# Optimization experiments

Hardware: AMD Instinct MI355X
Metric: run time of the kernel (lower is better)

The kernel has to match this reference:

```python
import jax, jax.numpy as jnp
import numpy as np
from jax import lax

B, T, H, Q = 32, 2000, 896, 256
SUB = H // 2


def wavrnn_normalize(x):
    return 2.0 * x / 255.0 - 1.0


def setup_inputs() -> dict:
    key = jax.random.key(0)
    ks = jax.random.split(key, 10)
    p = lambda k, shape: (jax.random.normal(k, shape, dtype=jnp.float32) * 0.02)
    return {
        "sample": jax.random.randint(ks[0], (B, T, 2), 0, 256, dtype=jnp.int32),
        "cts": jax.random.randint(ks[1], (B, T, 1), 0, 256, dtype=jnp.int32),
        "state": jnp.zeros((B, H), dtype=jnp.float32),
        "R": p(ks[2], (3 * H, H)),
        "Wc": p(ks[3], (3 * SUB, 2)),
        "Wf": p(ks[4], (3 * SUB, 3)),
        "b_u": jnp.zeros((H,), jnp.float32),
        "b_r": jnp.zeros((H,), jnp.float32),
        "b_e": jnp.zeros((H,), jnp.float32),
        "Wc1": p(ks[5], (SUB, SUB)),
        "bc1": jnp.zeros((SUB,), jnp.float32),
        "Wc2": p(ks[6], (Q, SUB)),
        "bc2": jnp.zeros((Q,), jnp.float32),
        "Wf1": p(ks[7], (SUB, SUB)),
        "bf1": jnp.zeros((SUB,), jnp.float32),
        "Wf2": p(ks[8], (Q, SUB)),
        "bf2": jnp.zeros((Q,), jnp.float32),
    }


def reference(sample, cts, state, R, Wc, Wf, b_u, b_r, b_e,
              Wc1, bc1, Wc2, bc2, Wf1, bf1, Wf2, bf2):
    s = wavrnn_normalize(sample.astype(jnp.float32))          # [B,T,2]
    c = wavrnn_normalize(cts.astype(jnp.float32))             # [B,T,1]
    s_f = jnp.concatenate([s, c], axis=2)                     # [B,T,3]

    proj_c = jnp.einsum('btk,ok->bto', s, Wc)                 # [B,T,3*SUB]
    proj_f = jnp.einsum('btk,ok->bto', s_f, Wf)               # [B,T,3*SUB]
    utc, rtc, etc_ = jnp.split(proj_c, 3, axis=2)
    utf, rtf, etf = jnp.split(proj_f, 3, axis=2)
    fwd_u = jnp.concatenate([utc, utf], axis=2)               # [B,T,H]
    fwd_r = jnp.concatenate([rtc, rtf], axis=2)
    fwd_e = jnp.concatenate([etc_, etf], axis=2)

    # time-major for scan: [T,B,H]
    xs = (jnp.swapaxes(fwd_u, 0, 1), jnp.swapaxes(fwd_r, 0, 1), jnp.swapaxes(fwd_e, 0, 1))

    def step(h, x):
        fu, fr, fe = x                                        # each [B,H]
        r_ = h @ R.T                                          # [B,3H]
        r_u, r_r, r_e = jnp.split(r_, 3, axis=1)
        ut = jax.nn.sigmoid(r_u + fu + b_u)
        rt = jax.nn.sigmoid(r_r + fr + b_r)
        et = jnp.tanh(rt * r_e + fe + b_e)
        h_new = ut * h + (1.0 - ut) * et
        return h_new, h_new

    last, states = lax.scan(step, state, xs)                  # states [T,B,H]
    states = jnp.swapaxes(states, 0, 1)                       # [B,T,H]
    htc, htf = jnp.split(states, 2, axis=2)                   # [B,T,SUB] each

    ct = jax.nn.log_softmax(
        jax.nn.relu(jnp.einsum('btk,ok->bto', htc, Wc1) + bc1) @ Wc2.T + bc2, axis=2)
    ft = jax.nn.log_softmax(
        jax.nn.relu(jnp.einsum('btk,ok->bto', htf, Wf1) + bf1) @ Wf2.T + bf2, axis=2)
    return (ct, ft, last[:, None, :])
```

## Files before the change

### kernel.cpp

```cpp
#include <hip/hip_runtime.h>
#include <hip/hip_bf16.h>

#define B_   32
#define T_   2000
#define H_   896
#define SUB_ 448
#define Q_   256

#define FT_OFF   16384000
#define LAST_OFF 32768000

#define NBLK_ 28

#define WS_FLAGS  0
#define WS_H0     8192
#define WS_WB     65536
#define WS_STATES 1327104

#define WB_W1C 0
#define WB_W1F 200704
#define WB_W2C 401408
#define WB_W2F 516096
#define WB_N   630784

#define SLOT_B 57344
#define SLOT_E 28672

typedef __attribute__((ext_vector_type(8)))  short bf16x8;
typedef __attribute__((ext_vector_type(16))) float f32x16;

__device__ __forceinline__ unsigned short f2bf(float f) {
    unsigned int u = __builtin_bit_cast(unsigned int, f);
    u += 0x7fff + ((u >> 16) & 1);
    return (unsigned short)(u >> 16);
}
__device__ __forceinline__ float bf2f(unsigned short u) {
    return __builtin_bit_cast(float, (unsigned int)u << 16);
}
__device__ __forceinline__ void gload_lds16(const void* g, void* l) {
    __builtin_amdgcn_global_load_lds(
        (const __attribute__((address_space(1))) unsigned int*)g,
        (__attribute__((address_space(3))) unsigned int*)l, 16, 0, 0);
}
__device__ __forceinline__ bf16x8 mk8(short4 a, short4 b) {
    bf16x8 f;
    f[0]=a.x; f[1]=a.y; f[2]=a.z; f[3]=a.w;
    f[4]=b.x; f[5]=b.y; f[6]=b.z; f[7]=b.w;
    return f;
}
__device__ __forceinline__ float fsig(float x) {
    return __builtin_amdgcn_rcpf(1.0f + __expf(-x));
}
__device__ __forceinline__ float ftanh(float x) {
    float xc = fminf(fmaxf(x, -9.0f), 9.0f);
    float z  = __expf(2.0f * xc);
    return 1.0f - 2.0f * __builtin_amdgcn_rcpf(z + 1.0f);
}

__global__ void wavrnn_prep(const float* __restrict__ state,
                            const float* __restrict__ Wc1, const float* __restrict__ Wf1,
                            const float* __restrict__ Wc2, const float* __restrict__ Wf2,
                            unsigned short* __restrict__ wb,
                            unsigned short* __restrict__ h0,
                            int* __restrict__ flags) {
    const int i = blockIdx.x * 256 + threadIdx.x;
    if (i < WB_N) {
        float v;
        if      (i < WB_W1F) v = Wc1[i];
        else if (i < WB_W2C) v = Wf1[i - WB_W1F];
        else if (i < WB_W2F) v = Wc2[i - WB_W2C];
        else                 v = Wf2[i - WB_W2F];
        wb[i] = f2bf(v);
    }
    if (i < 64) flags[i] = 0;
    if (i < B_ * H_) h0[i] = f2bf(state[i]);
}

__global__ __launch_bounds__(192, 1)
void wavrnn_scan8(const int* __restrict__ sample, const int* __restrict__ cts,
                  const float* __restrict__ state, const float* __restrict__ R,
                  const float* __restrict__ Wc, const float* __restrict__ Wf,
                  const float* __restrict__ b_u, const float* __restrict__ b_r,
                  const float* __restrict__ b_e,
                  const unsigned short* __restrict__ h0,
                  int* __restrict__ flags,
                  unsigned short* __restrict__ states,
                  float* __restrict__ out)
{
    const int tid  = (int)threadIdx.x;
    const int w    = tid >> 6;
    const int lane = tid & 63;
    const int s31  = lane & 31;
    const int hi   = lane >> 5;
    const int b    = (int)blockIdx.x;

    __shared__ __align__(16) char Abuf[32 * 2048];
    __shared__ float gate_out[3][32][34];

    const int jgB = b * 32 + s31;
    bf16x8 Bf[56];
    {
        const float* Rrow = R + (size_t)(w * H_ + jgB) * H_;
        #pragma unroll
        for (int c = 0; c < 56; ++c) {
            const float4 p0 = *(const float4*)(Rrow + 16*c + 4*hi);
            const float4 p1 = *(const float4*)(Rrow + 16*c + 8 + 4*hi);
            bf16x8 f;
            f[0]=(short)f2bf(p0.x); f[1]=(short)f2bf(p0.y);
            f[2]=(short)f2bf(p0.z); f[3]=(short)f2bf(p0.w);
            f[4]=(short)f2bf(p1.x); f[5]=(short)f2bf(p1.y);
            f[6]=(short)f2bf(p1.z); f[7]=(short)f2bf(p1.w);
            Bf[c] = f;
        }
    }

    const int jp  = tid & 15;
    const int sg  = (tid >> 4) & 7;
    const int j0  = 2 * jp;
    const int jg0 = b * 32 + j0;
    float wu[2][3], wr[2][3], we[2][3], gb[2][3];
    float hreg[4][2];
    if (tid < 128) {
        #pragma unroll
        for (int jj = 0; jj < 2; ++jj) {
            const int jg = jg0 + jj;
            if (jg < SUB_) {
                wu[jj][0]=Wc[2*jg];            wu[jj][1]=Wc[2*jg+1];            wu[jj][2]=0.f;
                wr[jj][0]=Wc[2*(SUB_+jg)];     wr[jj][1]=Wc[2*(SUB_+jg)+1];     wr[jj][2]=0.f;
                we[jj][0]=Wc[2*(2*SUB_+jg)];   we[jj][1]=Wc[2*(2*SUB_+jg)+1];   we[jj][2]=0.f;
            } else {
                const int jf = jg - SUB_;
                wu[jj][0]=Wf[3*jf];            wu[jj][1]=Wf[3*jf+1];            wu[jj][2]=Wf[3*jf+2];
                wr[jj][0]=Wf[3*(SUB_+jf)];     wr[jj][1]=Wf[3*(SUB_+jf)+1];     wr[jj][2]=Wf[3*(SUB_+jf)+2];
                we[jj][0]=Wf[3*(2*SUB_+jf)];   we[jj][1]=Wf[3*(2*SUB_+jf)+1];   we[jj][2]=Wf[3*(2*SUB_+jf)+2];
            }
            gb[jj][0]=b_u[jg]; gb[jj][1]=b_r[jg]; gb[jj][2]=b_e[jg];
        }
        #pragma unroll
        for (int q = 0; q < 4; ++q) {
            const int s = sg*4 + q;
            hreg[q][0] = state[(size_t)s*H_ + jg0];
            hreg[q][1] = state[(size_t)s*H_ + jg0 + 1];
        }
    }
    __syncthreads();

    const int v16l = lane * 16;
    const char* abb = Abuf + s31*2048 + 8*s31 + 8*hi;

    #pragma unroll 1
    for (int t = 1; t <= T_; ++t) {
        float s0n[4], s1n[4], c0n[4];
        if (tid < 128) {
            const float kn = 2.0f / 255.0f;
            #pragma unroll
            for (int q = 0; q < 4; ++q) {
                const size_t idx = (size_t)(sg*4 + q)*T_ + (size_t)(t - 1);
                const int2 sv = *(const int2*)(sample + idx*2);
                s0n[q] = kn*(float)sv.x - 1.0f;
                s1n[q] = kn*(float)sv.y - 1.0f;
                c0n[q] = kn*(float)cts[idx] - 1.0f;
            }
        }
        for (;;) {
            int v = (lane < NBLK_)
                ? __hip_atomic_load(&flags[lane], __ATOMIC_RELAXED, __HIP_MEMORY_SCOPE_AGENT)
                : 0x7fffffff;
            if (__all(v >= t - 1)) break;
        }
        asm volatile("" ::: "memory");
        __builtin_amdgcn_sched_barrier(0);

        {
            const char* sb = (t == 1) ? (const char*)h0
                                      : (const char*)states + (size_t)(t - 2)*SLOT_B;
            #pragma unroll
            for (int ii = 0; ii < 22; ++ii) {
                const int i = w + 3*ii;
                if (i < 64) {
                    const int sp   = i >> 1;
                    const int half = i & 1;
                    gload_lds16(sb + sp*1784 + half*1024 + v16l,
                                Abuf + sp*2048 + half*1024);
                }
            }
        }
        __syncthreads();

        f32x16 acc0, acc1;
        #pragma unroll
        for (int e = 0; e < 16; ++e) { acc0[e] = 0.0f; acc1[e] = 0.0f; }
        #pragma unroll
        for (int c2 = 0; c2 < 28; ++c2) {
            {
                const short4 p0 = *(const short4*)(abb + 64*c2);
                const short4 p1 = *(const short4*)(abb + 64*c2 + 16);
                acc0 = __builtin_amdgcn_mfma_f32_32x32x16_bf16(mk8(p0, p1), Bf[2*c2], acc0, 0, 0, 0);
            }
            {
                const short4 p0 = *(const short4*)(abb + 64*c2 + 32);
                const short4 p1 = *(const short4*)(abb + 64*c2 + 48);
                acc1 = __builtin_amdgcn_mfma_f32_32x32x16_bf16(mk8(p0, p1), Bf[2*c2+1], acc1, 0, 0, 0);
            }
        }
        #pragma unroll
        for (int e = 0; e < 16; ++e) {
            const int srow = (e & 3) + 8*(e >> 2) + 4*hi;
            gate_out[w][srow][s31] = acc0[e] + acc1[e];
        }
        __syncthreads();

        if (tid < 128) {
            #pragma unroll
            for (int q = 0; q < 4; ++q) {
                const int s = sg*4 + q;
                const float2 g0 = *(const float2*)&gate_out[0][s][j0];
                const float2 g1 = *(const float2*)&gate_out[1][s][j0];
                const float2 g2 = *(const float2*)&gate_out[2][s][j0];
                unsigned int packed = 0;
                #pragma unroll
                for (int jj = 0; jj < 2; ++jj) {
                    const float ru = jj ? g0.y : g0.x;
                    const float rr = jj ? g1.y : g1.x;
                    const float re = jj ? g2.y : g2.x;
                    const float fu = s0n[q]*wu[jj][0] + s1n[q]*wu[jj][1] + c0n[q]*wu[jj][2];
                    const float fr = s0n[q]*wr[jj][0] + s1n[q]*wr[jj][1] + c0n[q]*wr[jj][2];
                    const float fe = s0n[q]*we[jj][0] + s1n[q]*we[jj][1] + c0n[q]*we[jj][2];
                    const float ut = fsig(ru + fu + gb[jj][0]);
                    const float rt = fsig(rr + fr + gb[jj][1]);
                    const float et = ftanh(rt*re + fe + gb[jj][2]);
                    const float hn = ut*hreg[q][jj] + (1.0f - ut)*et;
                    hreg[q][jj] = hn;
                    packed |= (unsigned int)f2bf(hn) << (16*jj);
                    if (t == T_) out[LAST_OFF + (size_t)s*H_ + jg0 + jj] = hn;
                }
                __hip_atomic_store(
                    (unsigned int*)(states + (size_t)(t-1)*SLOT_E + s*H_ + jg0),
                    packed, __ATOMIC_RELAXED, __HIP_MEMORY_SCOPE_AGENT);
            }
        }
        __syncthreads();
        if (tid == 0)
            __hip_atomic_store(&flags[b], t, __ATOMIC_RELAXED, __HIP_MEMORY_SCOPE_AGENT);
    }
}

__global__ __launch_bounds__(256, 1)
void wavrnn_head3(const unsigned short* __restrict__ states,
                  const unsigned short* __restrict__ wb,
                  const float* __restrict__ bc1, const float* __restrict__ bc2,
                  const float* __restrict__ bf1, const float* __restrict__ bf2,
                  float* __restrict__ out)
{
    __shared__ __align__(16) char stL[32 * 1920];
    __shared__ __align__(16) char a1L[32 * 1920];

    const int tid  = (int)threadIdx.x;
    const int w    = tid >> 6;
    const int lane = tid & 63;
    const int nl   = lane & 31;
    const int hi   = lane >> 5;
    const int row0 = (int)blockIdx.x * 32;

    #pragma unroll
    for (int ii = 0; ii < 28; ++ii) {
        const int idx = ii*256 + tid;
        const int rp  = idx / 224;
        const int p   = idx - rp*224;
        const int r   = row0 + rp;
        const int sr  = r / 2000;
        const int tr  = r - sr*2000;
        const uint2 v = *(const uint2*)(states + (size_t)tr*SLOT_E + sr*H_ + p*4);
        *(uint2*)(stL + rp*1920 + 8*(rp & 15) + p*8) = v;
    }
    __syncthreads();

    {
        const char* apb = stL + nl*1920 + 8*(nl & 15) + 8*hi;
        #pragma unroll 1
        for (int tt = 0; tt < 7; ++tt) {
            const int nt   = tt*4 + w;
            const int head = nt >= 14;
            const int jt   = nt - head*14;
            const int orow = jt*32 + nl;
            const unsigned short* wrp = wb + (head ? WB_W1F : WB_W1C) + (size_t)orow*448;
            const float bias = (head ? bf1 : bc1)[orow];
            const int ko = head * 896;
            f32x16 acc;
            #pragma unroll
            for (int e = 0; e < 16; ++e) acc[e] = bias;
            #pragma unroll
            for (int c = 0; c < 28; ++c) {
                const short4 a0 = *(const short4*)(apb + ko + 32*c);
                const short4 a1 = *(const short4*)(apb + ko + 32*c + 16);
                const short4 b0 = *(const short4*)((const char*)wrp + 32*c + 8*hi);
                const short4 b1 = *(const short4*)((const char*)wrp + 32*c + 8*hi + 16);
                acc = __builtin_amdgcn_mfma_f32_32x32x16_bf16(mk8(a0, a1), mk8(b0, b1), acc, 0, 0, 0);
            }
            const int jg = head*448 + jt*32 + nl;
            #pragma unroll
            for (int e = 0; e < 16; ++e) {
                const int m2 = (e & 3) + 8*(e >> 2) + 4*hi;
                *(unsigned short*)(a1L + m2*1920 + 8*(m2 & 15) + 2*jg) =
                    f2bf(fmaxf(acc[e], 0.0f));
            }
        }
    }
    __syncthreads();

    {
        unsigned short* lg = (unsigned short*)stL;
        const char* apb = a1L + nl*1920 + 8*(nl & 15) + 8*hi;
        #pragma unroll 1
        for (int tt = 0; tt < 4; ++tt) {
            const int nt   = tt*4 + w;
            const int head = nt >= 8;
            const int ct   = (nt & 7)*32 + nl;
            const unsigned short* wrp = wb + (head ? WB_W2F : WB_W2C) + (size_t)ct*448;
            const float bias = (head ? bf2 : bc2)[ct];
            const int ko = head * 896;
            f32x16 acc;
            #pragma unroll
            for (int e = 0; e < 16; ++e) acc[e] = bias;
            #pragma unroll
            for (int c = 0; c < 28; ++c) {
                const short4 a0 = *(const short4*)(apb + ko + 32*c);
                const short4 a1 = *(const short4*)(apb + ko + 32*c + 16);
                const short4 b0 = *(const short4*)((const char*)wrp + 32*c + 8*hi);
                const short4 b1 = *(const short4*)((const char*)wrp + 32*c + 8*hi + 16);
                acc = __builtin_amdgcn_mfma_f32_32x32x16_bf16(mk8(a0, a1), mk8(b0, b1), acc, 0, 0, 0);
            }
            #pragma unroll
            for (int e = 0; e < 16; ++e) {
                const int m2 = (e & 3) + 8*(e >> 2) + 4*hi;
                lg[m2*520 + head*256 + (nt & 7)*32 + nl] = f2bf(acc[e]);
            }
        }
    }
    __syncthreads();

    {
        const unsigned short* lg = (const unsigned short*)stL;
        #pragma unroll 1
        for (int p = w; p < 64; p += 4) {
            const int hh = p >> 5;
            const int rr = p & 31;
            const ushort4 lv = *(const ushort4*)(lg + rr*520 + hh*256 + 4*lane);
            const float v0 = bf2f(lv.x), v1 = bf2f(lv.y), v2 = bf2f(lv.z), v3 = bf2f(lv.w);
            float m = fmaxf(fmaxf(v0, v1), fmaxf(v2, v3));
            #pragma unroll
            for (int d = 1; d < 64; d <<= 1) m = fmaxf(m, __shfl_xor(m, d));
            float sm = __expf(v0-m) + __expf(v1-m) + __expf(v2-m) + __expf(v3-m);
            #pragma unroll
            for (int d = 1; d < 64; d <<= 1) sm += __shfl_xor(sm, d);
            const float ls = m + __logf(sm);
            float* o = out + (hh ? (size_t)FT_OFF : (size_t)0) + (size_t)(row0 + rr)*Q_ + 4*lane;
            o[0] = v0 - ls; o[1] = v1 - ls; o[2] = v2 - ls; o[3] = v3 - ls;
        }
    }
}

extern "C" void kernel_launch(void* const* d_in, const int* in_sizes, int n_in,
                              void* d_out, int out_size, void* d_ws, size_t ws_size,
                              hipStream_t stream) {
    (void)in_sizes; (void)n_in; (void)out_size; (void)ws_size;
    const int*   sample = (const int*)d_in[0];
    const int*   cts    = (const int*)d_in[1];
    const float* state  = (const float*)d_in[2];
    const float* R      = (const float*)d_in[3];
    const float* Wc     = (const float*)d_in[4];
    const float* Wf     = (const float*)d_in[5];
    const float* b_u    = (const float*)d_in[6];
    const float* b_r    = (const float*)d_in[7];
    const float* b_e    = (const float*)d_in[8];
    const float* Wc1    = (const float*)d_in[9];
    const float* bc1    = (const float*)d_in[10];
    const float* Wc2    = (const float*)d_in[11];
    const float* bc2    = (const float*)d_in[12];
    const float* Wf1    = (const float*)d_in[13];
    const float* bf1    = (const float*)d_in[14];
    const float* Wf2    = (const float*)d_in[15];
    const float* bf2    = (const float*)d_in[16];

    float* out = (float*)d_out;
    int*            flags  = (int*)((char*)d_ws + WS_FLAGS);
    unsigned short* h0     = (unsigned short*)((char*)d_ws + WS_H0);
    unsigned short* wb     = (unsigned short*)((char*)d_ws + WS_WB);
    unsigned short* states = (unsigned short*)((char*)d_ws + WS_STATES);

    wavrnn_prep<<<2464, 256, 0, stream>>>(state, Wc1, Wf1, Wc2, Wf2, wb, h0, flags);
    wavrnn_scan8<<<NBLK_, 192, 0, stream>>>(sample, cts, state, R, Wc, Wf,
                                            b_u, b_r, b_e, h0, flags, states, out);
    wavrnn_head3<<<(B_ * T_) / 32, 256, 0, stream>>>(states, wb, bc1, bc2, bf1, bf2, out);
}
```

Measured before the change: 11.28 ms.

## Split batch into two half-groups to overlap recurrence MFMA with cross-block sync

The persistent scan kernel now processes the 32 batch rows as two independent groups of 16, each with its own flag array and LDS buffer. While one group's matmul runs, the other group's states from the previous step are polled and staged through registers into LDS. This hides the inter-block flag wait and global load latency behind compute. The cost is that each MFMA now uses only half its 32-row tile, which doubles MFMA issue per useful row, and the code needs more synchronisation logic and registers.

```diff
diff --git a/kernel.cpp b/kernel.cpp
--- a/kernel.cpp
+++ b/kernel.cpp
@@ -25,6 +25,7 @@
 
 #define SLOT_B 57344
 #define SLOT_E 28672
+#define GRP_B  28672
 
 typedef __attribute__((ext_vector_type(8)))  short bf16x8;
 typedef __attribute__((ext_vector_type(16))) float f32x16;
@@ -36,11 +37,6 @@
 }
 __device__ __forceinline__ float bf2f(unsigned short u) {
     return __builtin_bit_cast(float, (unsigned int)u << 16);
-}
-__device__ __forceinline__ void gload_lds16(const void* g, void* l) {
-    __builtin_amdgcn_global_load_lds(
-        (const __attribute__((address_space(1))) unsigned int*)g,
-        (__attribute__((address_space(3))) unsigned int*)l, 16, 0, 0);
 }
 __device__ __forceinline__ bf16x8 mk8(short4 a, short4 b) {
     bf16x8 f;
@@ -55,6 +51,16 @@
     float xc = fminf(fmaxf(x, -9.0f), 9.0f);
     float z  = __expf(2.0f * xc);
     return 1.0f - 2.0f * __builtin_amdgcn_rcpf(z + 1.0f);
+}
+__device__ __forceinline__ void lds_barrier() {
+    asm volatile("s_waitcnt lgkmcnt(0)" ::: "memory");
+    __builtin_amdgcn_sched_barrier(0);
+    __builtin_amdgcn_s_barrier();
+    __builtin_amdgcn_sched_barrier(0);
+}
+__device__ __forceinline__ void vm_drain() {
+    asm volatile("s_waitcnt vmcnt(0)" ::: "memory");
+    __builtin_amdgcn_sched_barrier(0);
 }
 
 __global__ void wavrnn_prep(const float* __restrict__ state,
@@ -77,13 +83,13 @@
 }
 
 __global__ __launch_bounds__(192, 1)
-void wavrnn_scan8(const int* __restrict__ sample, const int* __restrict__ cts,
+void wavrnn_scan9(const int* __restrict__ sample, const int* __restrict__ cts,
                   const float* __restrict__ state, const float* __restrict__ R,
                   const float* __restrict__ Wc, const float* __restrict__ Wf,
                   const float* __restrict__ b_u, const float* __restrict__ b_r,
                   const float* __restrict__ b_e,
                   const unsigned short* __restrict__ h0,
-                  int* __restrict__ flags,
+                  int* __restrict__ flagsA, int* __restrict__ flagsB,
                   unsigned short* __restrict__ states,
                   float* __restrict__ out)
 {
@@ -94,8 +100,9 @@
     const int hi   = lane >> 5;
     const int b    = (int)blockIdx.x;
 
-    __shared__ __align__(16) char Abuf[32 * 2048];
-    __shared__ float gate_out[3][32][34];
+    __shared__ __align__(16) char AbufA[16 * 2048];
+    __shared__ __align__(16) char AbufB[16 * 2048];
+    __shared__ float gate_out[3][16][34];
 
     const int jgB = b * 32 + s31;
     bf16x8 Bf[56];
@@ -115,11 +122,11 @@
     }
 
     const int jp  = tid & 15;
-    const int sg  = (tid >> 4) & 7;
+    const int sp  = (tid >> 4) & 7;
     const int j0  = 2 * jp;
     const int jg0 = b * 32 + j0;
     float wu[2][3], wr[2][3], we[2][3], gb[2][3];
-    float hreg[4][2];
+    float hregA[2][2], hregB[2][2];
     if (tid < 128) {
         #pragma unroll
         for (int jj = 0; jj < 2; ++jj) {
@@ -137,112 +144,163 @@
             gb[jj][0]=b_u[jg]; gb[jj][1]=b_r[jg]; gb[jj][2]=b_e[jg];
         }
         #pragma unroll
-        for (int q = 0; q < 4; ++q) {
-            const int s = sg*4 + q;
-            hreg[q][0] = state[(size_t)s*H_ + jg0];
-            hreg[q][1] = state[(size_t)s*H_ + jg0 + 1];
+        for (int q = 0; q < 2; ++q) {
+            hregA[q][0] = state[(size_t)(2*sp+q)*H_ + jg0];
+            hregA[q][1] = state[(size_t)(2*sp+q)*H_ + jg0 + 1];
+            hregB[q][0] = state[(size_t)(16+2*sp+q)*H_ + jg0];
+            hregB[q][1] = state[(size_t)(16+2*sp+q)*H_ + jg0 + 1];
+        }
+    }
+
+    const char* abbA = AbufA + (s31 & 15)*2048 + 8*(s31 & 15) + 8*hi;
+    const char* abbB = AbufB + (s31 & 15)*2048 + 8*(s31 & 15) + 8*hi;
+
+    {
+        const char* src = (const char*)h0;
+        #pragma unroll
+        for (int i = 0; i < 10; ++i) {
+            const int p = tid + 192*i;
+            if (p < 1792) {
+                const int s = p & 15, ww = p >> 4;
+                *(uint4*)(AbufA + s*2056 + 16*ww) = *(const uint4*)(src + s*1792 + 16*ww);
+            }
         }
     }
     __syncthreads();
 
-    const int v16l = lane * 16;
-    const char* abb = Abuf + s31*2048 + 8*s31 + 8*hi;
+#define MFMA_HALF(ABB)                                                          \
+    {                                                                            \
+        f32x16 acc0, acc1;                                                       \
+        _Pragma("unroll") for (int e = 0; e < 16; ++e) { acc0[e]=0.f; acc1[e]=0.f; } \
+        _Pragma("unroll") for (int c2 = 0; c2 < 28; ++c2) {                      \
+            const short4 p0 = *(const short4*)((ABB) + 64*c2);                   \
+            const short4 p1 = *(const short4*)((ABB) + 64*c2 + 16);              \
+            acc0 = __builtin_amdgcn_mfma_f32_32x32x16_bf16(mk8(p0,p1), Bf[2*c2],   acc0, 0,0,0); \
+            const short4 p2 = *(const short4*)((ABB) + 64*c2 + 32);              \
+            const short4 p3 = *(const short4*)((ABB) + 64*c2 + 48);              \
+            acc1 = __builtin_amdgcn_mfma_f32_32x32x16_bf16(mk8(p2,p3), Bf[2*c2+1], acc1, 0,0,0); \
+        }                                                                        \
+        _Pragma("unroll") for (int e = 0; e < 8; ++e) {                          \
+            const int srow = (e & 3) + 8*(e >> 2) + 4*hi;                        \
+            gate_out[w][srow][s31] = acc0[e] + acc1[e];                          \
+        }                                                                        \
+    }
+
+#define POLL(FL, NEED)                                                           \
+    {                                                                            \
+        for (;;) {                                                               \
+            int v = (lane < NBLK_)                                               \
+                ? __hip_atomic_load(&(FL)[lane], __ATOMIC_RELAXED, __HIP_MEMORY_SCOPE_AGENT) \
+                : 0x7fffffff;                                                    \
+            if (__all(v >= (NEED))) break;                                       \
+        }                                                                        \
+        __builtin_amdgcn_sched_barrier(0);                                       \
+    }
+
+#define INPUTS(GSBASE, TT)                                                       \
+    float s0n[2], s1n[2], c0n[2];                                                \
+    if (tid < 128) {                                                             \
+        const float kn = 2.0f / 255.0f;                                          \
+        _Pragma("unroll") for (int q = 0; q < 2; ++q) {                          \
+            const size_t idx = (size_t)((GSBASE) + 2*sp + q)*T_ + (size_t)((TT) - 1); \
+            const int2 sv = *(const int2*)(sample + idx*2);                      \
+            s0n[q] = kn*(float)sv.x - 1.0f;                                      \
+            s1n[q] = kn*(float)sv.y - 1.0f;                                      \
+            c0n[q] = kn*(float)cts[idx] - 1.0f;                                  \
+        }                                                                        \
+    }
+
+#define STAGE_LOAD(SRC)                                                          \
+    _Pragma("unroll") for (int i = 0; i < 10; ++i) {                             \
+        const int p = tid + 192*i;                                               \
+        if (p < 1792) {                                                          \
+            const int s = p & 15, ww = p >> 4;                                   \
+            rg[i] = *(const uint4*)((SRC) + s*1792 + 16*ww);                     \
+        }                                                                        \
+    }
+
+#define STAGE_WRITE(DST)                                                         \
+    _Pragma("unroll") for (int i = 0; i < 10; ++i) {                             \
+        const int p = tid + 192*i;                                               \
+        if (p < 1792) {                                                          \
+            const int s = p & 15, ww = p >> 4;                                   \
+            *(uint4*)((DST) + s*2056 + 16*ww) = rg[i];                           \
+        }                                                                        \
+    }
+
+#define GATES_HALF(HREG, GSBASE, TT)                                             \
+    if (tid < 128) {                                                             \
+        _Pragma("unroll") for (int q = 0; q < 2; ++q) {                          \
+            const int sl = 2*sp + q;                                             \
+            const int gs = (GSBASE) + sl;                                        \
+            const float2 g0 = *(const float2*)&gate_out[0][sl][j0];              \
+            const float2 g1 = *(const float2*)&gate_out[1][sl][j0];              \
+            const float2 g2 = *(const float2*)&gate_out[2][sl][j0];              \
+            unsigned int packed = 0;                                             \
+            _Pragma("unroll") for (int jj = 0; jj < 2; ++jj) {                   \
+                const float ru = jj ? g0.y : g0.x;                               \
+                const float rr = jj ? g1.y : g1.x;                               \
+                const float re = jj ? g2.y : g2.x;                               \
+                const float fu = s0n[q]*wu[jj][0] + s1n[q]*wu[jj][1] + c0n[q]*wu[jj][2]; \
+                const float fr = s0n[q]*wr[jj][0] + s1n[q]*wr[jj][1] + c0n[q]*wr[jj][2]; \
+                const float fe = s0n[q]*we[jj][0] + s1n[q]*we[jj][1] + c0n[q]*we[jj][2]; \
+                const float ut = fsig(ru + fu + gb[jj][0]);                      \
+                const float rt = fsig(rr + fr + gb[jj][1]);                      \
+                const float et = ftanh(rt*re + fe + gb[jj][2]);                  \
+                const float hn = ut*(HREG)[q][jj] + (1.0f - ut)*et;              \
+                (HREG)[q][jj] = hn;                                              \
+                packed |= (unsigned int)f2bf(hn) << (16*jj);                     \
+                if ((TT) == T_) out[LAST_OFF + (size_t)gs*H_ + jg0 + jj] = hn;   \
+            }                                                                    \
+            __hip_atomic_store(                                                  \
+                (unsigned int*)(states + (size_t)((TT)-1)*SLOT_E + gs*H_ + jg0), \
+                packed, __ATOMIC_RELAXED, __HIP_MEMORY_SCOPE_AGENT);             \
+        }                                                                        \
+    }
 
     #pragma unroll 1
     for (int t = 1; t <= T_; ++t) {
-        float s0n[4], s1n[4], c0n[4];
-        if (tid < 128) {
-            const float kn = 2.0f / 255.0f;
-            #pragma unroll
-            for (int q = 0; q < 4; ++q) {
-                const size_t idx = (size_t)(sg*4 + q)*T_ + (size_t)(t - 1);
-                const int2 sv = *(const int2*)(sample + idx*2);
-                s0n[q] = kn*(float)sv.x - 1.0f;
-                s1n[q] = kn*(float)sv.y - 1.0f;
-                c0n[q] = kn*(float)cts[idx] - 1.0f;
-            }
-        }
-        for (;;) {
-            int v = (lane < NBLK_)
-                ? __hip_atomic_load(&flags[lane], __ATOMIC_RELAXED, __HIP_MEMORY_SCOPE_AGENT)
-                : 0x7fffffff;
-            if (__all(v >= t - 1)) break;
-        }
-        asm volatile("" ::: "memory");
-        __builtin_amdgcn_sched_barrier(0);
-
         {
-            const char* sb = (t == 1) ? (const char*)h0
-                                      : (const char*)states + (size_t)(t - 2)*SLOT_B;
-            #pragma unroll
-            for (int ii = 0; ii < 22; ++ii) {
-                const int i = w + 3*ii;
-                if (i < 64) {
-                    const int sp   = i >> 1;
-                    const int half = i & 1;
-                    gload_lds16(sb + sp*1784 + half*1024 + v16l,
-                                Abuf + sp*2048 + half*1024);
-                }
-            }
-        }
-        __syncthreads();
-
-        f32x16 acc0, acc1;
-        #pragma unroll
-        for (int e = 0; e < 16; ++e) { acc0[e] = 0.0f; acc1[e] = 0.0f; }
-        #pragma unroll
-        for (int c2 = 0; c2 < 28; ++c2) {
-            {
-                const short4 p0 = *(const short4*)(abb + 64*c2);
-                const short4 p1 = *(const short4*)(abb + 64*c2 + 16);
-                acc0 = __builtin_amdgcn_mfma_f32_32x32x16_bf16(mk8(p0, p1), Bf[2*c2], acc0, 0, 0, 0);
-            }
-            {
-                const short4 p0 = *(const short4*)(abb + 64*c2 + 32);
-                const short4 p1 = *(const short4*)(abb + 64*c2 + 48);
-                acc1 = __builtin_amdgcn_mfma_f32_32x32x16_bf16(mk8(p0, p1), Bf[2*c2+1], acc1, 0, 0, 0);
-            }
-        }
-        #pragma unroll
-        for (int e = 0; e < 16; ++e) {
-            const int srow = (e & 3) + 8*(e >> 2) + 4*hi;
-            gate_out[w][srow][s31] = acc0[e] + acc1[e];
-        }
-        __syncthreads();
-
-        if (tid < 128) {
-            #pragma unroll
-            for (int q = 0; q < 4; ++q) {
-                const int s = sg*4 + q;
-                const float2 g0 = *(const float2*)&gate_out[0][s][j0];
-                const float2 g1 = *(const float2*)&gate_out[1][s][j0];
-                const float2 g2 = *(const float2*)&gate_out[2][s][j0];
-                unsigned int packed = 0;
-                #pragma unroll
-                for (int jj = 0; jj < 2; ++jj) {
-                    const float ru = jj ? g0.y : g0.x;
-                    const float rr = jj ? g1.y : g1.x;
-                    const float re = jj ? g2.y : g2.x;
-                    const float fu = s0n[q]*wu[jj][0] + s1n[q]*wu[jj][1] + c0n[q]*wu[jj][2];
-                    const float fr = s0n[q]*wr[jj][0] + s1n[q]*wr[jj][1] + c0n[q]*wr[jj][2];
-                    const float fe = s0n[q]*we[jj][0] + s1n[q]*we[jj][1] + c0n[q]*we[jj][2];
-                    const float ut = fsig(ru + fu + gb[jj][0]);
-                    const float rt = fsig(rr + fr + gb[jj][1]);
-                    const float et = ftanh(rt*re + fe + gb[jj][2]);
-                    const float hn = ut*hreg[q][jj] + (1.0f - ut)*et;
-                    hreg[q][jj] = hn;
-                    packed |= (unsigned int)f2bf(hn) << (16*jj);
-                    if (t == T_) out[LAST_OFF + (size_t)s*H_ + jg0 + jj] = hn;
-                }
-                __hip_atomic_store(
-                    (unsigned int*)(states + (size_t)(t-1)*SLOT_E + s*H_ + jg0),
-                    packed, __ATOMIC_RELAXED, __HIP_MEMORY_SCOPE_AGENT);
-            }
-        }
-        __syncthreads();
-        if (tid == 0)
-            __hip_atomic_store(&flags[b], t, __ATOMIC_RELAXED, __HIP_MEMORY_SCOPE_AGENT);
-    }
+            MFMA_HALF(abbA);
+            INPUTS(0, t);
+            POLL(flagsB, t - 1);
+            uint4 rg[10];
+            const char* srcB = (t == 1)
+                ? (const char*)h0 + GRP_B
+                : (const char*)states + (size_t)(t - 2)*SLOT_B + GRP_B;
+            STAGE_LOAD(srcB);
+            lds_barrier();
+            GATES_HALF(hregA, 0, t);
+            STAGE_WRITE(AbufB);
+            vm_drain();
+            lds_barrier();
+            if (tid == 0)
+                __hip_atomic_store(&flagsA[b], t, __ATOMIC_RELAXED, __HIP_MEMORY_SCOPE_AGENT);
+        }
+        {
+            MFMA_HALF(abbB);
+            INPUTS(16, t);
+            uint4 rg[10];
+            if (t < T_) {
+                POLL(flagsA, t);
+                const char* srcA = (const char*)states + (size_t)(t - 1)*SLOT_B;
+                STAGE_LOAD(srcA);
+            }
+            lds_barrier();
+            GATES_HALF(hregB, 16, t);
+            if (t < T_) { STAGE_WRITE(AbufA); }
+            vm_drain();
+            lds_barrier();
+            if (tid == 0)
+                __hip_atomic_store(&flagsB[b], t, __ATOMIC_RELAXED, __HIP_MEMORY_SCOPE_AGENT);
+        }
+    }
+#undef MFMA_HALF
+#undef POLL
+#undef INPUTS
+#undef STAGE_LOAD
+#undef STAGE_WRITE
+#undef GATES_HALF
 }
 
 __global__ __launch_bounds__(256, 1)
@@ -383,13 +441,14 @@
     const float* bf2    = (const float*)d_in[16];
 
     float* out = (float*)d_out;
-    int*            flags  = (int*)((char*)d_ws + WS_FLAGS);
+    int*            flagsA = (int*)((char*)d_ws + WS_FLAGS);
+    int*            flagsB = (int*)((char*)d_ws + WS_FLAGS + 128);
     unsigned short* h0     = (unsigned short*)((char*)d_ws + WS_H0);
     unsigned short* wb     = (unsigned short*)((char*)d_ws + WS_WB);
     unsigned short* states = (unsigned short*)((char*)d_ws + WS_STATES);
 
-    wavrnn_prep<<<2464, 256, 0, stream>>>(state, Wc1, Wf1, Wc2, Wf2, wb, h0, flags);
-    wavrnn_scan8<<<NBLK_, 192, 0, stream>>>(sample, cts, state, R, Wc, Wf,
-                                            b_u, b_r, b_e, h0, flags, states, out);
+    wavrnn_prep<<<2464, 256, 0, stream>>>(state, Wc1, Wf1, Wc2, Wf2, wb, h0, flagsA);
+    wavrnn_scan9<<<NBLK_, 192, 0, stream>>>(sample, cts, state, R, Wc, Wf,
+                                            b_u, b_r, b_e, h0, flagsA, flagsB, states, out);
     wavrnn_head3<<<(B_ * T_) / 32, 256, 0, stream>>>(states, wb, bc1, bc2, bf1, bf2, out);
 }
```

After: 31.46 ms. 2.79x slower.

## Replace per-step flag barrier with NaN-sentinel polling on state data

Applied to the files above, without the earlier changes.

Removes the per-block step flags and the end-of-step block barrier. Consumers instead poll the hidden-state buffer directly and treat a bf16 NaN pair as not yet written. A new kernel pre-fills the whole states buffer with that sentinel, and state rows are now copied into shared memory through registers with atomic loads rather than async global-to-LDS loads. This is meant to cut the flag round-trip latency on the serial 2000-step critical path. In exchange it adds a roughly 115MB fill pass, and it breaks if a real hidden value ever equals the sentinel bit pattern.

```diff
diff --git a/kernel.cpp b/kernel.cpp
--- a/kernel.cpp
+++ b/kernel.cpp
@@ -25,6 +25,7 @@
 
 #define SLOT_B 57344
 #define SLOT_E 28672
+#define NAN2   0x7FC07FC0u
 
 typedef __attribute__((ext_vector_type(8)))  short bf16x8;
 typedef __attribute__((ext_vector_type(16))) float f32x16;
@@ -36,11 +37,6 @@
 }
 __device__ __forceinline__ float bf2f(unsigned short u) {
     return __builtin_bit_cast(float, (unsigned int)u << 16);
-}
-__device__ __forceinline__ void gload_lds16(const void* g, void* l) {
-    __builtin_amdgcn_global_load_lds(
-        (const __attribute__((address_space(1))) unsigned int*)g,
-        (__attribute__((address_space(3))) unsigned int*)l, 16, 0, 0);
 }
 __device__ __forceinline__ bf16x8 mk8(short4 a, short4 b) {
     bf16x8 f;
@@ -57,12 +53,16 @@
     return 1.0f - 2.0f * __builtin_amdgcn_rcpf(z + 1.0f);
 }
 
+__global__ void wavrnn_nanfill(uint4* __restrict__ states4) {
+    const size_t i = (size_t)blockIdx.x * 256 + threadIdx.x;
+    if (i < 7168000u) states4[i] = uint4{NAN2, NAN2, NAN2, NAN2};
+}
+
 __global__ void wavrnn_prep(const float* __restrict__ state,
                             const float* __restrict__ Wc1, const float* __restrict__ Wf1,
                             const float* __restrict__ Wc2, const float* __restrict__ Wf2,
                             unsigned short* __restrict__ wb,
-                            unsigned short* __restrict__ h0,
-                            int* __restrict__ flags) {
+                            unsigned short* __restrict__ h0) {
     const int i = blockIdx.x * 256 + threadIdx.x;
     if (i < WB_N) {
         float v;
@@ -72,20 +72,18 @@
         else                 v = Wf2[i - WB_W2F];
         wb[i] = f2bf(v);
     }
-    if (i < 64) flags[i] = 0;
     if (i < B_ * H_) h0[i] = f2bf(state[i]);
 }
 
 __global__ __launch_bounds__(192, 1)
-void wavrnn_scan8(const int* __restrict__ sample, const int* __restrict__ cts,
-                  const float* __restrict__ state, const float* __restrict__ R,
-                  const float* __restrict__ Wc, const float* __restrict__ Wf,
-                  const float* __restrict__ b_u, const float* __restrict__ b_r,
-                  const float* __restrict__ b_e,
-                  const unsigned short* __restrict__ h0,
-                  int* __restrict__ flags,
-                  unsigned short* __restrict__ states,
-                  float* __restrict__ out)
+void wavrnn_scan10(const int* __restrict__ sample, const int* __restrict__ cts,
+                   const float* __restrict__ state, const float* __restrict__ R,
+                   const float* __restrict__ Wc, const float* __restrict__ Wf,
+                   const float* __restrict__ b_u, const float* __restrict__ b_r,
+                   const float* __restrict__ b_e,
+                   const unsigned short* __restrict__ h0,
+                   unsigned short* __restrict__ states,
+                   float* __restrict__ out)
 {
     const int tid  = (int)threadIdx.x;
     const int w    = tid >> 6;
@@ -145,7 +143,6 @@
     }
     __syncthreads();
 
-    const int v16l = lane * 16;
     const char* abb = Abuf + s31*2048 + 8*s31 + 8*hi;
 
     #pragma unroll 1
@@ -162,26 +159,53 @@
                 c0n[q] = kn*(float)cts[idx] - 1.0f;
             }
         }
-        for (;;) {
-            int v = (lane < NBLK_)
-                ? __hip_atomic_load(&flags[lane], __ATOMIC_RELAXED, __HIP_MEMORY_SCOPE_AGENT)
-                : 0x7fffffff;
-            if (__all(v >= t - 1)) break;
-        }
-        asm volatile("" ::: "memory");
-        __builtin_amdgcn_sched_barrier(0);
 
         {
-            const char* sb = (t == 1) ? (const char*)h0
-                                      : (const char*)states + (size_t)(t - 2)*SLOT_B;
-            #pragma unroll
-            for (int ii = 0; ii < 22; ++ii) {
-                const int i = w + 3*ii;
-                if (i < 64) {
-                    const int sp   = i >> 1;
-                    const int half = i & 1;
-                    gload_lds16(sb + sp*1784 + half*1024 + v16l,
-                                Abuf + sp*2048 + half*1024);
+            uint4 va[19];
+            unsigned int todo = (tid < 128) ? 0x7FFFFu : 0x3FFFFu;
+            if (t == 1) {
+                const char* sb = (const char*)h0;
+                #pragma unroll
+                for (int i = 0; i < 19; ++i) {
+                    const int p = tid + 192*i;
+                    if (p < 3584) {
+                        const int r = p / 112, c = p - r*112;
+                        va[i] = *(const uint4*)(sb + r*1792 + c*16);
+                    }
+                }
+            } else {
+                const unsigned int* sbd =
+                    (const unsigned int*)((const char*)states + (size_t)(t - 2)*SLOT_B);
+                #pragma unroll 1
+                while (todo) {
+                    #pragma unroll
+                    for (int i = 0; i < 19; ++i) {
+                        if (todo & (1u << i)) {
+                            const int p = tid + 192*i;
+                            const int r = p / 112, c = p - r*112;
+                            const unsigned int* s = sbd + r*448 + c*4;
+                            va[i].x = __hip_atomic_load(s+0, __ATOMIC_RELAXED, __HIP_MEMORY_SCOPE_AGENT);
+                            va[i].y = __hip_atomic_load(s+1, __ATOMIC_RELAXED, __HIP_MEMORY_SCOPE_AGENT);
+                            va[i].z = __hip_atomic_load(s+2, __ATOMIC_RELAXED, __HIP_MEMORY_SCOPE_AGENT);
+                            va[i].w = __hip_atomic_load(s+3, __ATOMIC_RELAXED, __HIP_MEMORY_SCOPE_AGENT);
+                        }
+                    }
+                    #pragma unroll
+                    for (int i = 0; i < 19; ++i) {
+                        if (todo & (1u << i)) {
+                            if ((va[i].x != NAN2) & (va[i].y != NAN2) &
+                                (va[i].z != NAN2) & (va[i].w != NAN2))
+                                todo &= ~(1u << i);
+                        }
+                    }
+                }
+            }
+            #pragma unroll
+            for (int i = 0; i < 19; ++i) {
+                const int p = tid + 192*i;
+                if (p < 3584) {
+                    const int r = p / 112, c = p - r*112;
+                    *(uint4*)(Abuf + r*2056 + c*16) = va[i];
                 }
             }
         }
@@ -239,9 +263,6 @@
                     packed, __ATOMIC_RELAXED, __HIP_MEMORY_SCOPE_AGENT);
             }
         }
-        __syncthreads();
-        if (tid == 0)
-            __hip_atomic_store(&flags[b], t, __ATOMIC_RELAXED, __HIP_MEMORY_SCOPE_AGENT);
     }
 }
 
@@ -383,13 +404,13 @@
     const float* bf2    = (const float*)d_in[16];
 
     float* out = (float*)d_out;
-    int*            flags  = (int*)((char*)d_ws + WS_FLAGS);
     unsigned short* h0     = (unsigned short*)((char*)d_ws + WS_H0);
     unsigned short* wb     = (unsigned short*)((char*)d_ws + WS_WB);
     unsigned short* states = (unsigned short*)((char*)d_ws + WS_STATES);
 
-    wavrnn_prep<<<2464, 256, 0, stream>>>(state, Wc1, Wf1, Wc2, Wf2, wb, h0, flags);
-    wavrnn_scan8<<<NBLK_, 192, 0, stream>>>(sample, cts, state, R, Wc, Wf,
-                                            b_u, b_r, b_e, h0, flags, states, out);
+    wavrnn_nanfill<<<28000, 256, 0, stream>>>((uint4*)states);
+    wavrnn_prep<<<2464, 256, 0, stream>>>(state, Wc1, Wf1, Wc2, Wf2, wb, h0);
+    wavrnn_scan10<<<NBLK_, 192, 0, stream>>>(sample, cts, state, R, Wc, Wf,
+                                             b_u, b_r, b_e, h0, states, out);
     wavrnn_head3<<<(B_ * T_) / 32, 256, 0, stream>>>(states, wb, bc1, bc2, bf1, bf2, out);
 }
```

New measurement: 20.35 ms. 1.8x slower.
